# Performance work log

Hardware: AMD Instinct MI355X
Metric: run time of the kernel (lower is better)

## Reference

```python
import jax, jax.numpy as jnp
import numpy as np

EPS = 1e-8

def _skew(v):
    x, y, z = v[..., 0], v[..., 1], v[..., 2]
    o = jnp.zeros_like(x)
    return jnp.stack([
        jnp.stack([o, -z, y], -1),
        jnp.stack([z, o, -x], -1),
        jnp.stack([-y, x, o], -1)], -2)

def _theta(phi):
    t2 = jnp.sum(phi * phi, -1)
    small = t2 < EPS
    t2s = jnp.where(small, 1.0, t2)  # safe for division / sqrt grads
    th = jnp.sqrt(t2s)
    return t2, t2s, th, small

def so3_exp(phi):
    # Rodrigues formula with small-angle Taylor branches
    t2, t2s, th, small = _theta(phi)
    A = jnp.where(small, 1.0 - t2 / 6.0, jnp.sin(th) / th)
    B = jnp.where(small, 0.5 - t2 / 24.0, (1.0 - jnp.cos(th)) / t2s)
    K = _skew(phi)
    I = jnp.eye(3, dtype=phi.dtype)
    return I + A[..., None, None] * K + B[..., None, None] * (K @ K)

def so3_left_jac(phi):
    t2, t2s, th, small = _theta(phi)
    B = jnp.where(small, 0.5 - t2 / 24.0, (1.0 - jnp.cos(th)) / t2s)
    C = jnp.where(small, 1.0 / 6.0 - t2 / 120.0, (th - jnp.sin(th)) / (t2s * th))
    K = _skew(phi)
    I = jnp.eye(3, dtype=phi.dtype)
    return I + B[..., None, None] * K + C[..., None, None] * (K @ K)

def so3_inv_left_jac(phi):
    t2, t2s, th, small = _theta(phi)
    D = jnp.where(small, 1.0 / 12.0 + t2 / 720.0,
                  1.0 / t2s - (1.0 + jnp.cos(th)) / (2.0 * th * jnp.sin(th)))
    K = _skew(phi)
    I = jnp.eye(3, dtype=phi.dtype)
    return I - 0.5 * K + D[..., None, None] * (K @ K)

def so3_log(R):
    tr = R[..., 0, 0] + R[..., 1, 1] + R[..., 2, 2]
    c = jnp.clip(0.5 * (tr - 1.0), -1.0 + 1e-7, 1.0 - 1e-7)
    th = jnp.arccos(c)                       # th in (~4.5e-4, pi), never exactly 0
    factor = th / (2.0 * jnp.sin(th))        # -> 0.5 as th -> 0
    vee = jnp.stack([R[..., 2, 1] - R[..., 1, 2],
                     R[..., 0, 2] - R[..., 2, 0],
                     R[..., 1, 0] - R[..., 0, 1]], -1)
    return factor[..., None] * vee

def se3_exp(xi):
    # xi = [rho, phi]
    rho, phi = xi[..., :3], xi[..., 3:]
    R = so3_exp(phi)
    t = jnp.einsum('...ij,...j->...i', so3_left_jac(phi), rho)
    top = jnp.concatenate([R, t[..., None]], -1)                      # [...,3,4]
    bot = jnp.broadcast_to(jnp.array([0.0, 0.0, 0.0, 1.0], dtype=xi.dtype),
                           xi.shape[:-1] + (1, 4))
    return jnp.concatenate([top, bot], -2)                            # [...,4,4]

def se3_log(T):
    R = T[..., :3, :3]
    t = T[..., :3, 3]
    phi = so3_log(R)
    rho = jnp.einsum('...ij,...j->...i', so3_inv_left_jac(phi), t)
    return jnp.concatenate([rho, phi], -1)                            # [...,6]

def setup_inputs() -> dict:
    key = jax.random.key(0)
    k1, k2, k3 = jax.random.split(key, 3)
    B = 500000
    inp = 0.5 * jax.random.normal(k1, (B, 6), dtype=jnp.float32)
    target_xi = 0.5 * jax.random.normal(k2, (B, 6), dtype=jnp.float32)
    target_T_inv = se3_exp(target_xi)                                 # valid SE(3) mats
    A = jax.random.normal(k3, (6, 6), dtype=jnp.float32)
    precision = A @ A.T / 6.0 + jnp.eye(6, dtype=jnp.float32)         # SPD info matrix
    return {"input": inp, "target_T_inv": target_T_inv, "precision": precision}

def reference(input, target_T_inv, precision):
    B = input.shape[0]
    xi_star = se3_log(target_T_inv)                                   # [B,6]
    g_xi = se3_log(se3_exp(input) @ target_T_inv)                     # [B,6]
    # trace(X @ P @ X^T) == sum_b x_b^T P x_b ; never materialize [B,B]
    quad = lambda X: jnp.einsum('bi,ij,bj->', X, precision, X)
    loss = (0.5 / B) * (quad(g_xi) - quad(xi_star))
    return loss.reshape(1)
```

## Files before the change

kernel.cpp:

```cpp
#include <hip/hip_runtime.h>
#include <math.h>

__device__ __forceinline__ float frcp(float x) { return __builtin_amdgcn_rcpf(x); }

__device__ __forceinline__ float acos_fast(float x) {
    float a = fabsf(x);
    float p = fmaf(a, fmaf(a, fmaf(a, -0.0187293f, 0.0742610f), -0.2121144f), 1.5707288f);
    float r = sqrtf(1.0f - a) * p;
    return x >= 0.0f ? r : 3.14159274f - r;
}

__device__ __forceinline__ void se3_log_fast(const float R[9], const float t[3], float xi[6]) {
    float tr = R[0] + R[4] + R[8];
    float c = 0.5f * (tr - 1.0f);
    c = fminf(fmaxf(c, -1.0f + 1e-7f), 1.0f - 1e-7f);
    float th = acos_fast(c);
    float s2 = sqrtf(fmaxf(1.0f - c * c, 0.0f));
    float factor = th * frcp(2.0f * s2);

    float p0 = factor * (R[7] - R[5]);
    float p1 = factor * (R[2] - R[6]);
    float p2 = factor * (R[3] - R[1]);

    float xx = p0 * p0, yy = p1 * p1, zz = p2 * p2;
    float xy = p0 * p1, xz = p0 * p2, yz = p1 * p2;
    float t2 = xx + yy + zz;

    bool small = t2 < 1e-6f;
    float D = small ? (1.0f / 12.0f + t2 * (1.0f / 720.0f))
                    : (frcp(t2) - (1.0f + c) * frcp(2.0f * th * s2));

    float J00 = 1.0f - D * (yy + zz);
    float J01 = 0.5f * p2 + D * xy;
    float J02 = -0.5f * p1 + D * xz;
    float J10 = -0.5f * p2 + D * xy;
    float J11 = 1.0f - D * (xx + zz);
    float J12 = 0.5f * p0 + D * yz;
    float J20 = 0.5f * p1 + D * xz;
    float J21 = -0.5f * p0 + D * yz;
    float J22 = 1.0f - D * (xx + yy);

    xi[0] = J00 * t[0] + J01 * t[1] + J02 * t[2];
    xi[1] = J10 * t[0] + J11 * t[1] + J12 * t[2];
    xi[2] = J20 * t[0] + J21 * t[1] + J22 * t[2];
    xi[3] = p0;
    xi[4] = p1;
    xi[5] = p2;
}

__global__ __launch_bounds__(256) void se3_loss_kernel(
    const float* __restrict__ inp,
    const float* __restrict__ tgt,
    const float* __restrict__ prec,
    float* __restrict__ out, int n)
{
    __shared__ float wsum[4];
    int tid = threadIdx.x;

    float acc = 0.0f;
    int i = blockIdx.x * 256 + tid;
    if (i < n) {
        const float2* xi2 = (const float2*)(inp + 6 * (size_t)i);
        float2 a0 = xi2[0], a1 = xi2[1], a2 = xi2[2];
        float r0 = a0.x, r1 = a0.y, r2 = a1.x;
        float p0 = a1.y, p1 = a2.x, p2 = a2.y;

        const float4* T4 = (const float4*)(tgt + 16 * (size_t)i);
        float4 row0 = T4[0], row1 = T4[1], row2 = T4[2];
        float Rt[9] = { row0.x, row0.y, row0.z,
                        row1.x, row1.y, row1.z,
                        row2.x, row2.y, row2.z };
        float tt[3] = { row0.w, row1.w, row2.w };

        float sx[6];
        se3_log_fast(Rt, tt, sx);

        float xx = p0 * p0, yy = p1 * p1, zz = p2 * p2;
        float xy = p0 * p1, xz = p0 * p2, yz = p1 * p2;
        float t2 = xx + yy + zz;
        bool small = t2 < 1e-8f;
        float t2s = small ? 1.0f : t2;
        float th = sqrtf(t2s);
        float s  = __sinf(th);
        float cth = __cosf(th);
        float rth = frcp(th);
        float rt2s = frcp(t2s);
        float A  = small ? (1.0f - t2 * (1.0f / 6.0f))  : (s * rth);
        float Bv = small ? (0.5f - t2 * (1.0f / 24.0f)) : ((1.0f - cth) * rt2s);
        float Cv = small ? (1.0f / 6.0f - t2 * (1.0f / 120.0f)) : ((th - s) * rt2s * rth);

        float R00 = 1.0f - Bv * (yy + zz);
        float R01 = -A * p2 + Bv * xy;
        float R02 =  A * p1 + Bv * xz;
        float R10 =  A * p2 + Bv * xy;
        float R11 = 1.0f - Bv * (xx + zz);
        float R12 = -A * p0 + Bv * yz;
        float R20 = -A * p1 + Bv * xz;
        float R21 =  A * p0 + Bv * yz;
        float R22 = 1.0f - Bv * (xx + yy);

        float J00 = 1.0f - Cv * (yy + zz);
        float J01 = -Bv * p2 + Cv * xy;
        float J02 =  Bv * p1 + Cv * xz;
        float J10 =  Bv * p2 + Cv * xy;
        float J11 = 1.0f - Cv * (xx + zz);
        float J12 = -Bv * p0 + Cv * yz;
        float J20 = -Bv * p1 + Cv * xz;
        float J21 =  Bv * p0 + Cv * yz;
        float J22 = 1.0f - Cv * (xx + yy);

        float t0 = J00 * r0 + J01 * r1 + J02 * r2;
        float t1 = J10 * r0 + J11 * r1 + J12 * r2;
        float t3 = J20 * r0 + J21 * r1 + J22 * r2;

        float MR[9], Mt[3];
        MR[0] = R00 * Rt[0] + R01 * Rt[3] + R02 * Rt[6];
        MR[1] = R00 * Rt[1] + R01 * Rt[4] + R02 * Rt[7];
        MR[2] = R00 * Rt[2] + R01 * Rt[5] + R02 * Rt[8];
        MR[3] = R10 * Rt[0] + R11 * Rt[3] + R12 * Rt[6];
        MR[4] = R10 * Rt[1] + R11 * Rt[4] + R12 * Rt[7];
        MR[5] = R10 * Rt[2] + R11 * Rt[5] + R12 * Rt[8];
        MR[6] = R20 * Rt[0] + R21 * Rt[3] + R22 * Rt[6];
        MR[7] = R20 * Rt[1] + R21 * Rt[4] + R22 * Rt[7];
        MR[8] = R20 * Rt[2] + R21 * Rt[5] + R22 * Rt[8];
        Mt[0] = R00 * tt[0] + R01 * tt[1] + R02 * tt[2] + t0;
        Mt[1] = R10 * tt[0] + R11 * tt[1] + R12 * tt[2] + t1;
        Mt[2] = R20 * tt[0] + R21 * tt[1] + R22 * tt[2] + t3;

        float g[6];
        se3_log_fast(MR, Mt, g);

        float d[6], e[6];
        #pragma unroll
        for (int ii = 0; ii < 6; ii++) { d[ii] = g[ii] - sx[ii]; e[ii] = g[ii] + sx[ii]; }
        #pragma unroll
        for (int ii = 0; ii < 6; ii++) {
            float pe = 0.0f;
            #pragma unroll
            for (int jj = 0; jj < 6; jj++)
                pe = fmaf(prec[ii * 6 + jj], e[jj], pe);
            acc = fmaf(d[ii], pe, acc);
        }
    }

    #pragma unroll
    for (int off = 32; off > 0; off >>= 1)
        acc += __shfl_down(acc, off);
    int lane = tid & 63, w = tid >> 6;
    if (lane == 0) wsum[w] = acc;
    __syncthreads();
    if (tid == 0) {
        float bsum = wsum[0] + wsum[1] + wsum[2] + wsum[3];
        atomicAdd(out, bsum * (0.5f / (float)n));
    }
}

extern "C" void kernel_launch(void* const* d_in, const int* in_sizes, int n_in,
                              void* d_out, int out_size, void* d_ws, size_t ws_size,
                              hipStream_t stream) {
    const float* inp  = (const float*)d_in[0];
    const float* tgt  = (const float*)d_in[1];
    const float* prec = (const float*)d_in[2];
    float* out = (float*)d_out;
    int n = in_sizes[0] / 6;

    int block = 256;
    int grid = (n + block - 1) / block;
    se3_loss_kernel<<<grid, block, 0, stream>>>(inp, tgt, prec, out, n);
}
```

Measured before the change: 103.7 us.

## Grid-stride loop with register prefetch of next element's inputs

Turns the one-element-per-thread kernel into a grid-stride loop over roughly two elements per thread, halving the grid. The loads for the next element are issued before computing the current one so memory latency overlaps with the per-element math. This also halves the number of block reductions and atomics. The cost is extra registers for the prefetched values and fewer waves in flight to hide latency.

```diff
diff --git a/kernel.cpp b/kernel.cpp
--- a/kernel.cpp
+++ b/kernel.cpp
@@ -48,6 +48,83 @@
     xi[5] = p2;
 }
 
+__device__ __forceinline__ float elem_contrib(
+    float r0, float r1, float r2, float p0, float p1, float p2,
+    const float Rt[9], const float tt[3], const float* __restrict__ prec)
+{
+    float sx[6];
+    se3_log_fast(Rt, tt, sx);
+
+    float xx = p0 * p0, yy = p1 * p1, zz = p2 * p2;
+    float xy = p0 * p1, xz = p0 * p2, yz = p1 * p2;
+    float t2 = xx + yy + zz;
+    bool small = t2 < 1e-8f;
+    float t2s = small ? 1.0f : t2;
+    float th = sqrtf(t2s);
+    float s  = __sinf(th);
+    float cth = __cosf(th);
+    float rth = frcp(th);
+    float rt2s = frcp(t2s);
+    float A  = small ? (1.0f - t2 * (1.0f / 6.0f))  : (s * rth);
+    float Bv = small ? (0.5f - t2 * (1.0f / 24.0f)) : ((1.0f - cth) * rt2s);
+    float Cv = small ? (1.0f / 6.0f - t2 * (1.0f / 120.0f)) : ((th - s) * rt2s * rth);
+
+    float R00 = 1.0f - Bv * (yy + zz);
+    float R01 = -A * p2 + Bv * xy;
+    float R02 =  A * p1 + Bv * xz;
+    float R10 =  A * p2 + Bv * xy;
+    float R11 = 1.0f - Bv * (xx + zz);
+    float R12 = -A * p0 + Bv * yz;
+    float R20 = -A * p1 + Bv * xz;
+    float R21 =  A * p0 + Bv * yz;
+    float R22 = 1.0f - Bv * (xx + yy);
+
+    float J00 = 1.0f - Cv * (yy + zz);
+    float J01 = -Bv * p2 + Cv * xy;
+    float J02 =  Bv * p1 + Cv * xz;
+    float J10 =  Bv * p2 + Cv * xy;
+    float J11 = 1.0f - Cv * (xx + zz);
+    float J12 = -Bv * p0 + Cv * yz;
+    float J20 = -Bv * p1 + Cv * xz;
+    float J21 =  Bv * p0 + Cv * yz;
+    float J22 = 1.0f - Cv * (xx + yy);
+
+    float t0 = J00 * r0 + J01 * r1 + J02 * r2;
+    float t1 = J10 * r0 + J11 * r1 + J12 * r2;
+    float t3 = J20 * r0 + J21 * r1 + J22 * r2;
+
+    float MR[9], Mt[3];
+    MR[0] = R00 * Rt[0] + R01 * Rt[3] + R02 * Rt[6];
+    MR[1] = R00 * Rt[1] + R01 * Rt[4] + R02 * Rt[7];
+    MR[2] = R00 * Rt[2] + R01 * Rt[5] + R02 * Rt[8];
+    MR[3] = R10 * Rt[0] + R11 * Rt[3] + R12 * Rt[6];
+    MR[4] = R10 * Rt[1] + R11 * Rt[4] + R12 * Rt[7];
+    MR[5] = R10 * Rt[2] + R11 * Rt[5] + R12 * Rt[8];
+    MR[6] = R20 * Rt[0] + R21 * Rt[3] + R22 * Rt[6];
+    MR[7] = R20 * Rt[1] + R21 * Rt[4] + R22 * Rt[7];
+    MR[8] = R20 * Rt[2] + R21 * Rt[5] + R22 * Rt[8];
+    Mt[0] = R00 * tt[0] + R01 * tt[1] + R02 * tt[2] + t0;
+    Mt[1] = R10 * tt[0] + R11 * tt[1] + R12 * tt[2] + t1;
+    Mt[2] = R20 * tt[0] + R21 * tt[1] + R22 * tt[2] + t3;
+
+    float g[6];
+    se3_log_fast(MR, Mt, g);
+
+    float d[6], e[6];
+    #pragma unroll
+    for (int ii = 0; ii < 6; ii++) { d[ii] = g[ii] - sx[ii]; e[ii] = g[ii] + sx[ii]; }
+    float q = 0.0f;
+    #pragma unroll
+    for (int ii = 0; ii < 6; ii++) {
+        float pe = 0.0f;
+        #pragma unroll
+        for (int jj = 0; jj < 6; jj++)
+            pe = fmaf(prec[ii * 6 + jj], e[jj], pe);
+        q = fmaf(d[ii], pe, q);
+    }
+    return q;
+}
+
 __global__ __launch_bounds__(256) void se3_loss_kernel(
     const float* __restrict__ inp,
     const float* __restrict__ tgt,
@@ -56,91 +133,38 @@
 {
     __shared__ float wsum[4];
     int tid = threadIdx.x;
+    int stride = gridDim.x * 256;
+    int i = blockIdx.x * 256 + tid;
+    float acc = 0.0f;
 
-    float acc = 0.0f;
-    int i = blockIdx.x * 256 + tid;
-    if (i < n) {
+    bool valid = i < n;
+    float2 a0, a1, a2; float4 w0, w1, w2;
+    if (valid) {
         const float2* xi2 = (const float2*)(inp + 6 * (size_t)i);
-        float2 a0 = xi2[0], a1 = xi2[1], a2 = xi2[2];
-        float r0 = a0.x, r1 = a0.y, r2 = a1.x;
-        float p0 = a1.y, p1 = a2.x, p2 = a2.y;
+        a0 = xi2[0]; a1 = xi2[1]; a2 = xi2[2];
+        const float4* T4 = (const float4*)(tgt + 16 * (size_t)i);
+        w0 = T4[0]; w1 = T4[1]; w2 = T4[2];
+    }
+    while (valid) {
+        int inext = i + stride;
+        bool vnext = inext < n;
+        float2 b0, b1, b2; float4 x0, x1, x2;
+        if (vnext) {
+            const float2* xi2 = (const float2*)(inp + 6 * (size_t)inext);
+            b0 = xi2[0]; b1 = xi2[1]; b2 = xi2[2];
+            const float4* T4 = (const float4*)(tgt + 16 * (size_t)inext);
+            x0 = T4[0]; x1 = T4[1]; x2 = T4[2];
+        }
 
-        const float4* T4 = (const float4*)(tgt + 16 * (size_t)i);
-        float4 row0 = T4[0], row1 = T4[1], row2 = T4[2];
-        float Rt[9] = { row0.x, row0.y, row0.z,
-                        row1.x, row1.y, row1.z,
-                        row2.x, row2.y, row2.z };
-        float tt[3] = { row0.w, row1.w, row2.w };
+        float Rt[9] = { w0.x, w0.y, w0.z,
+                        w1.x, w1.y, w1.z,
+                        w2.x, w2.y, w2.z };
+        float tt[3] = { w0.w, w1.w, w2.w };
+        acc += elem_contrib(a0.x, a0.y, a1.x, a1.y, a2.x, a2.y, Rt, tt, prec);
 
-        float sx[6];
-        se3_log_fast(Rt, tt, sx);
-
-        float xx = p0 * p0, yy = p1 * p1, zz = p2 * p2;
-        float xy = p0 * p1, xz = p0 * p2, yz = p1 * p2;
-        float t2 = xx + yy + zz;
-        bool small = t2 < 1e-8f;
-        float t2s = small ? 1.0f : t2;
-        float th = sqrtf(t2s);
-        float s  = __sinf(th);
-        float cth = __cosf(th);
-        float rth = frcp(th);
-        float rt2s = frcp(t2s);
-        float A  = small ? (1.0f - t2 * (1.0f / 6.0f))  : (s * rth);
-        float Bv = small ? (0.5f - t2 * (1.0f / 24.0f)) : ((1.0f - cth) * rt2s);
-        float Cv = small ? (1.0f / 6.0f - t2 * (1.0f / 120.0f)) : ((th - s) * rt2s * rth);
-
-        float R00 = 1.0f - Bv * (yy + zz);
-        float R01 = -A * p2 + Bv * xy;
-        float R02 =  A * p1 + Bv * xz;
-        float R10 =  A * p2 + Bv * xy;
-        float R11 = 1.0f - Bv * (xx + zz);
-        float R12 = -A * p0 + Bv * yz;
-        float R20 = -A * p1 + Bv * xz;
-        float R21 =  A * p0 + Bv * yz;
-        float R22 = 1.0f - Bv * (xx + yy);
-
-        float J00 = 1.0f - Cv * (yy + zz);
-        float J01 = -Bv * p2 + Cv * xy;
-        float J02 =  Bv * p1 + Cv * xz;
-        float J10 =  Bv * p2 + Cv * xy;
-        float J11 = 1.0f - Cv * (xx + zz);
-        float J12 = -Bv * p0 + Cv * yz;
-        float J20 = -Bv * p1 + Cv * xz;
-        float J21 =  Bv * p0 + Cv * yz;
-        float J22 = 1.0f - Cv * (xx + yy);
-
-        float t0 = J00 * r0 + J01 * r1 + J02 * r2;
-        float t1 = J10 * r0 + J11 * r1 + J12 * r2;
-        float t3 = J20 * r0 + J21 * r1 + J22 * r2;
-
-        float MR[9], Mt[3];
-        MR[0] = R00 * Rt[0] + R01 * Rt[3] + R02 * Rt[6];
-        MR[1] = R00 * Rt[1] + R01 * Rt[4] + R02 * Rt[7];
-        MR[2] = R00 * Rt[2] + R01 * Rt[5] + R02 * Rt[8];
-        MR[3] = R10 * Rt[0] + R11 * Rt[3] + R12 * Rt[6];
-        MR[4] = R10 * Rt[1] + R11 * Rt[4] + R12 * Rt[7];
-        MR[5] = R10 * Rt[2] + R11 * Rt[5] + R12 * Rt[8];
-        MR[6] = R20 * Rt[0] + R21 * Rt[3] + R22 * Rt[6];
-        MR[7] = R20 * Rt[1] + R21 * Rt[4] + R22 * Rt[7];
-        MR[8] = R20 * Rt[2] + R21 * Rt[5] + R22 * Rt[8];
-        Mt[0] = R00 * tt[0] + R01 * tt[1] + R02 * tt[2] + t0;
-        Mt[1] = R10 * tt[0] + R11 * tt[1] + R12 * tt[2] + t1;
-        Mt[2] = R20 * tt[0] + R21 * tt[1] + R22 * tt[2] + t3;
-
-        float g[6];
-        se3_log_fast(MR, Mt, g);
-
-        float d[6], e[6];
-        #pragma unroll
-        for (int ii = 0; ii < 6; ii++) { d[ii] = g[ii] - sx[ii]; e[ii] = g[ii] + sx[ii]; }
-        #pragma unroll
-        for (int ii = 0; ii < 6; ii++) {
-            float pe = 0.0f;
-            #pragma unroll
-            for (int jj = 0; jj < 6; jj++)
-                pe = fmaf(prec[ii * 6 + jj], e[jj], pe);
-            acc = fmaf(d[ii], pe, acc);
-        }
+        a0 = b0; a1 = b1; a2 = b2;
+        w0 = x0; w1 = x1; w2 = x2;
+        i = inext; valid = vnext;
     }
 
     #pragma unroll
@@ -165,6 +189,7 @@
     int n = in_sizes[0] / 6;
 
     int block = 256;
-    int grid = (n + block - 1) / block;
+    int grid = (n + 2 * block - 1) / (2 * block);
+    if (grid < 1) grid = 1;
     se3_loss_kernel<<<grid, block, 0, stream>>>(inp, tgt, prec, out, n);
 }
```

Result: faster. 93.18 us (-10.2%).
